# Optimization experiments

Hardware: AMD Instinct MI355X
Metric: run time of the kernel (lower is better)

The kernel has to match this reference:

```python
import jax, jax.numpy as jnp
import numpy as np

B, D_IN, H = 8192, 4096, 128
E, N, C = 3, 256, 32          # experts, codebook_size, codebook_dim
D1, D2 = 512, 256             # down_units
U1, U2 = 256, 512             # up_units
CW = 0.25                     # commitment_weight


def setup_inputs() -> dict:
    key = jax.random.key(0)
    ks = jax.random.split(key, 16)
    s = 0.02
    f32 = jnp.float32
    inp = {
        'x':   jax.random.normal(ks[0], (B, D_IN), f32),
        # llm_down MLP: 4096 -> 512 -> 256 -> 128 (ReLU on hiddens, linear out)
        'Wd1': jax.random.normal(ks[1], (D_IN, D1), f32) * s, 'bd1': jnp.zeros((D1,), f32),
        'Wd2': jax.random.normal(ks[2], (D1, D2), f32) * s,  'bd2': jnp.zeros((D2,), f32),
        'Wd3': jax.random.normal(ks[3], (D2, H), f32) * s,   'bd3': jnp.zeros((H,), f32),
        # per-expert VQ: project_in 128->32, codebook [256,32], project_out 32->128
        'Win':  jax.random.normal(ks[4], (E, H, C), f32) * s, 'bin_': jnp.zeros((E, C), f32),
        'codebook': jax.random.normal(ks[5], (E, N, C), f32),
        'Wout': jax.random.normal(ks[6], (E, C, H), f32) * s, 'bout': jnp.zeros((E, H), f32),
        # llm_up MLP: 128 -> 256 -> 512 -> 4096
        'Wu1': jax.random.normal(ks[7], (H, U1), f32) * s,   'bu1': jnp.zeros((U1,), f32),
        'Wu2': jax.random.normal(ks[8], (U1, U2), f32) * s,  'bu2': jnp.zeros((U2,), f32),
        'Wu3': jax.random.normal(ks[9], (U2, D_IN), f32) * s, 'bu3': jnp.zeros((D_IN,), f32),
    }
    return inp


def _decorrelation_loss(qemb):
    # qemb: [B, E, H]
    b, e, h = qemb.shape
    cen = qemb - qemb.mean(axis=0, keepdims=True)
    cen = cen.transpose(1, 0, 2).reshape(e, -1)          # [E, B*H]
    cov = (cen @ cen.T) / (b * h - 1)                    # [E, E]
    std = jnp.sqrt(jnp.diag(cov))
    std = jnp.where(std > 1e-8, std, 1.0)
    corr = cov / jnp.outer(std, std)
    c2 = corr ** 2
    return c2.sum() - jnp.diag(c2).sum()


def _vq_experts(latent, Win, bin_, codebook, Wout, bout):
    # latent: [B,H]; all experts share the same (unmasked) latent.
    xe = jnp.einsum('bh,ehc->ebc', latent, Win) + bin_[:, None, :]      # [E,B,C]
    d2 = ((xe ** 2).sum(-1)[..., None]
          - 2.0 * jnp.einsum('ebc,enc->ebn', xe, codebook)
          + (codebook ** 2).sum(-1)[:, None, :])                        # [E,B,N]
    idx = jnp.argmin(d2, axis=-1)                                       # [E,B]
    q = jax.vmap(lambda c, i: c[i])(codebook, idx)                      # [E,B,C] gather
    commit = CW * jnp.mean((jax.lax.stop_gradient(q) - xe) ** 2, axis=(1, 2)).sum()
    quant = xe + jax.lax.stop_gradient(q - xe)                          # straight-through
    qe = jnp.einsum('ebc,ech->ebh', quant, Wout) + bout[:, None, :]     # [E,B,H]
    return qe, idx, commit


def reference(x, Wd1, bd1, Wd2, bd2, Wd3, bd3, Win, bin_, codebook, Wout, bout,
              Wu1, bu1, Wu2, bu2, Wu3, bu3):
    h = jax.nn.relu(x @ Wd1 + bd1)
    h = jax.nn.relu(h @ Wd2 + bd2)
    latent = h @ Wd3 + bd3                                              # [B,128]
    qe, idx, total_commit = _vq_experts(latent, Win, bin_, codebook, Wout, bout)
    qemb = qe.transpose(1, 0, 2)                                        # [B,E,H]
    decorr = _decorrelation_loss(qemb)
    rl = qemb.mean(axis=1)                                              # [B,H]
    u = jax.nn.relu(rl @ Wu1 + bu1)
    u = jax.nn.relu(u @ Wu2 + bu2)
    recon = jnp.clip(u @ Wu3 + bu3, -1.0, 1.0)                          # [B,4096]
    return (recon, idx.T, total_commit, decorr)
```

## Files before the change

kernel.cpp:

```cpp
#include <hip/hip_runtime.h>
#include <hip/hip_bf16.h>

using bf16 = __hip_bfloat16;

typedef __bf16 bf16x8 __attribute__((ext_vector_type(8)));
typedef float  f32x4  __attribute__((ext_vector_type(4)));
typedef unsigned long long u64;
typedef unsigned short u16;
typedef unsigned int u32;

__device__ __forceinline__ float b2f(bf16 v) { return __bfloat162float(v); }
__device__ __forceinline__ bf16  f2b(float v) { return __float2bfloat16(v); }
__device__ __forceinline__ u16   bits(bf16 v) { return __builtin_bit_cast(u16, v); }

static constexpr size_t SZ_WD1S = 512ull  * 12288 * 2;
static constexpr size_t SZ_WD2S = 256ull  * 1536  * 2;
static constexpr size_t SZ_WFUS = 128ull  * 768   * 2;
static constexpr size_t SZ_WU1T = 256ull  * 128   * 2;
static constexpr size_t SZ_WU2T = 512ull  * 256   * 2;
static constexpr size_t SZ_WU3T = 4096ull * 512   * 2;
static constexpr size_t SZ_H1S  = 8192ull * 1536  * 2;
static constexpr size_t SZ_H2S  = 8192ull * 768   * 2;
static constexpr size_t SZ_XE   = 8192ull * 128   * 4;
static constexpr size_t SZ_QEMB = 3ull * 8192 * 128 * 4;
static constexpr size_t SZ_RL   = 8192ull * 128   * 2;
static constexpr size_t SZ_U1   = 8192ull * 256   * 2;
static constexpr size_t SZ_U2   = 8192ull * 512   * 2;
static constexpr size_t SZ_CNRM = 768ull * 4;
static constexpr size_t SZ_BFUS = 128ull * 4;
static constexpr size_t SZ_PART = 4ull * 8192 * 512 * 4;

static constexpr size_t OFF_WD1S = 0;
static constexpr size_t OFF_WD2S = OFF_WD1S + SZ_WD1S;
static constexpr size_t OFF_WFUS = OFF_WD2S + SZ_WD2S;
static constexpr size_t OFF_WU1T = OFF_WFUS + SZ_WFUS;
static constexpr size_t OFF_WU2T = OFF_WU1T + SZ_WU1T;
static constexpr size_t OFF_WU3T = OFF_WU2T + SZ_WU2T;
static constexpr size_t OFF_H1S  = OFF_WU3T + SZ_WU3T;
static constexpr size_t OFF_H2S  = OFF_H1S  + SZ_H1S;
static constexpr size_t OFF_XE   = OFF_H2S  + SZ_H2S;
static constexpr size_t OFF_QEMB = OFF_XE   + SZ_XE;
static constexpr size_t OFF_RL   = OFF_QEMB + SZ_QEMB;
static constexpr size_t OFF_U1   = OFF_RL   + SZ_RL;
static constexpr size_t OFF_U2   = OFF_U1   + SZ_U1;
static constexpr size_t OFF_CNRM = OFF_U2   + SZ_U2;
static constexpr size_t OFF_BFUS = OFF_CNRM + ((SZ_CNRM + 255) & ~size_t(255));
static constexpr size_t OFF_STAT = OFF_BFUS + ((SZ_BFUS + 255) & ~size_t(255));
static constexpr size_t OFF_PART = OFF_STAT + 2048;

__global__ void wtrans_bf16(const float* __restrict__ in, bf16* __restrict__ out,
                            int K, int N)
{
    __shared__ float tile[32][33];
    const int tx = threadIdx.x, ty = threadIdx.y;
    const int n0 = blockIdx.x * 32, k0 = blockIdx.y * 32;
    #pragma unroll
    for (int i = 0; i < 32; i += 8)
        tile[ty + i][tx] = in[(size_t)(k0 + ty + i) * N + n0 + tx];
    __syncthreads();
    #pragma unroll
    for (int i = 0; i < 32; i += 8)
        out[(size_t)(n0 + ty + i) * K + k0 + tx] = f2b(tile[tx][ty + i]);
}

__global__ void wtrans_split3(const float* __restrict__ in, bf16* __restrict__ out,
                              int K, int N)
{
    __shared__ float tile[32][33];
    const int tx = threadIdx.x, ty = threadIdx.y;
    const int n0 = blockIdx.x * 32, k0 = blockIdx.y * 32;
    #pragma unroll
    for (int i = 0; i < 32; i += 8)
        tile[ty + i][tx] = in[(size_t)(k0 + ty + i) * N + n0 + tx];
    __syncthreads();
    #pragma unroll
    for (int i = 0; i < 32; i += 8) {
        const float v = tile[tx][ty + i];
        const bf16 hi = f2b(v);
        const bf16 lo = f2b(v - b2f(hi));
        bf16* o = out + (size_t)(n0 + ty + i) * 3 * K + 3 * (k0 + tx);
        o[0] = hi; o[1] = lo; o[2] = hi;
    }
}

__global__ void cnorm_kernel(const float* __restrict__ cb, float* __restrict__ cnorm)
{
    const int i = blockIdx.x * blockDim.x + threadIdx.x;
    if (i < 768) {
        float s = 0.f;
        for (int k = 0; k < 32; ++k) { const float v = cb[i * 32 + k]; s += v * v; }
        cnorm[i] = s;
    }
}

__global__ __launch_bounds__(256)
void wfuse_kernel(const float* __restrict__ Wd3, const float* __restrict__ bd3,
                  const float* __restrict__ Win, const float* __restrict__ bin_,
                  bf16* __restrict__ BtS, float* __restrict__ bfuse)
{
    const int n = blockIdx.x;
    const int t = threadIdx.x;
    if (n >= 96) {
        bf16* o = BtS + (size_t)n * 768 + 3 * t;
        o[0] = f2b(0.f); o[1] = f2b(0.f); o[2] = f2b(0.f);
        if (t == 0) bfuse[n] = 0.f;
        return;
    }
    const int e = n >> 5, c = n & 31;
    float s = 0.f;
    for (int h = 0; h < 128; ++h)
        s += Wd3[t * 128 + h] * Win[(size_t)(e * 128 + h) * 32 + c];
    const bf16 hi = f2b(s);
    const bf16 lo = f2b(s - b2f(hi));
    bf16* o = BtS + (size_t)n * 768 + 3 * t;
    o[0] = hi; o[1] = lo; o[2] = hi;
    if (t == 0) {
        float b = bin_[e * 32 + c];
        for (int h = 0; h < 128; ++h)
            b += bd3[h] * Win[(size_t)(e * 128 + h) * 32 + c];
        bfuse[n] = b;
    }
}

__global__ __launch_bounds__(256)
void gemm1_x3(const float* __restrict__ A, const bf16* __restrict__ Bs3,
              float* __restrict__ part)
{
    __shared__ bf16 As[128 * 96];
    __shared__ bf16 Bs[128 * 96];
    const int t = threadIdx.x, lane = t & 63, w = t >> 6;
    const int n0 = blockIdx.x * 128;
    const int m0 = blockIdx.y * 128;
    const int kz = blockIdx.z;
    const int wr = w >> 1, wc = w & 1, l15 = lane & 15, quad = lane >> 4;

    f32x4 acc[4][4];
    #pragma unroll
    for (int i = 0; i < 4; ++i)
        #pragma unroll
        for (int j = 0; j < 4; ++j)
            #pragma unroll
            for (int r = 0; r < 4; ++r) acc[i][j][r] = 0.f;

    const int kend = kz * 1024 + 1024;
    for (int ko = kz * 1024; ko < kend; ko += 32) {
        #pragma unroll
        for (int i = 0; i < 6; ++i) {
            const int c   = i * 256 + t;
            const int row = c / 12;
            const int cc  = c - row * 12;
            const bf16* gb = Bs3 + (size_t)(n0 + row) * 12288 + ko * 3 + cc * 8;
            __builtin_amdgcn_global_load_lds(
                (const __attribute__((address_space(1))) void*)gb,
                (__attribute__((address_space(3))) void*)(Bs + (size_t)c * 8), 16, 0, 0);
        }
        #pragma unroll
        for (int i = 0; i < 4; ++i) {
            const int c = i * 256 + t;
            const int row = c >> 3, c4 = c & 7;
            const float4 v = *(const float4*)(A + (size_t)(m0 + row) * 4096 + ko + c4 * 4);
            const float va[4] = {v.x, v.y, v.z, v.w};
            u64 h[4], l[4];
            #pragma unroll
            for (int j = 0; j < 4; ++j) {
                const bf16 hh = f2b(va[j]);
                h[j] = bits(hh);
                l[j] = bits(f2b(va[j] - b2f(hh)));
            }
            const u64 p0 = h[0] | (h[0] << 16) | (l[0] << 32) | (h[1] << 48);
            const u64 p1 = h[1] | (l[1] << 16) | (h[2] << 32) | (h[2] << 48);
            const u64 p2 = l[2] | (h[3] << 16) | (h[3] << 32) | (l[3] << 48);
            u64* dst = (u64*)(As + (size_t)row * 96 + c4 * 12);
            dst[0] = p0; dst[1] = p1; dst[2] = p2;
        }
        __syncthreads();
        #pragma unroll
        for (int kk = 0; kk < 3; ++kk) {
            bf16x8 af[4], bfr[4];
            #pragma unroll
            for (int mi = 0; mi < 4; ++mi)
                af[mi] = *(const bf16x8*)(As + (wr * 64 + mi * 16 + l15) * 96 + kk * 32 + quad * 8);
            #pragma unroll
            for (int ni = 0; ni < 4; ++ni)
                bfr[ni] = *(const bf16x8*)(Bs + (wc * 64 + ni * 16 + l15) * 96 + kk * 32 + quad * 8);
            #pragma unroll
            for (int mi = 0; mi < 4; ++mi)
                #pragma unroll
                for (int ni = 0; ni < 4; ++ni)
                    acc[mi][ni] = __builtin_amdgcn_mfma_f32_16x16x32_bf16(
                        af[mi], bfr[ni], acc[mi][ni], 0, 0, 0);
        }
        __syncthreads();
    }

    float* op = part + (size_t)kz * (8192ull * 512);
    #pragma unroll
    for (int mi = 0; mi < 4; ++mi)
        #pragma unroll
        for (int ni = 0; ni < 4; ++ni) {
            const int col = n0 + wc * 64 + ni * 16 + l15;
            #pragma unroll
            for (int r = 0; r < 4; ++r) {
                const int row = m0 + wr * 64 + mi * 16 + quad * 4 + r;
                op[(size_t)row * 512 + col] = acc[mi][ni][r];
            }
        }
}

__global__ __launch_bounds__(256)
void h1_epi(const float* __restrict__ part, const float* __restrict__ bias,
            bf16* __restrict__ out)
{
    const int idx = blockIdx.x * 256 + threadIdx.x;
    const int r = idx >> 7, c4 = idx & 127;
    const size_t base = (size_t)r * 512 + c4 * 4;
    const float4 p0 = *(const float4*)(part + 0ull * 8192 * 512 + base);
    const float4 p1 = *(const float4*)(part + 1ull * 8192 * 512 + base);
    const float4 p2 = *(const float4*)(part + 2ull * 8192 * 512 + base);
    const float4 p3 = *(const float4*)(part + 3ull * 8192 * 512 + base);
    const float4 bv = *(const float4*)(bias + c4 * 4);
    float v[4];
    v[0] = p0.x + p1.x + p2.x + p3.x + bv.x;
    v[1] = p0.y + p1.y + p2.y + p3.y + bv.y;
    v[2] = p0.z + p1.z + p2.z + p3.z + bv.z;
    v[3] = p0.w + p1.w + p2.w + p3.w + bv.w;
    u64 h[4], l[4];
    #pragma unroll
    for (int j = 0; j < 4; ++j) {
        const float vv = v[j] > 0.f ? v[j] : 0.f;
        const bf16 hi = f2b(vv);
        h[j] = bits(hi);
        l[j] = bits(f2b(vv - b2f(hi)));
    }
    const u64 w0 = h[0] | (h[0] << 16) | (l[0] << 32) | (h[1] << 48);
    const u64 w1 = h[1] | (l[1] << 16) | (h[2] << 32) | (h[2] << 48);
    const u64 w2 = l[2] | (h[3] << 16) | (h[3] << 32) | (l[3] << 48);
    u64* dst = (u64*)(out + (size_t)r * 1536 + 12 * c4);
    dst[0] = w0; dst[1] = w1; dst[2] = w2;
}

template <int EPI, int RELU>
__global__ __launch_bounds__(256)
void gemm_bt(const bf16* __restrict__ A, const bf16* __restrict__ Bt,
             const float* __restrict__ bias, void* __restrict__ outp,
             int M, int N, int K)
{
    __shared__ bf16 As[128 * 64];
    __shared__ bf16 Bs[128 * 64];
    const int t = threadIdx.x, lane = t & 63, w = t >> 6;
    const int n0 = blockIdx.x * 128;
    const int m0 = blockIdx.y * 128;
    const int wr = w >> 1, wc = w & 1, l15 = lane & 15, quad = lane >> 4;

    f32x4 acc[4][4];
    #pragma unroll
    for (int i = 0; i < 4; ++i)
        #pragma unroll
        for (int j = 0; j < 4; ++j)
            #pragma unroll
            for (int r = 0; r < 4; ++r) acc[i][j][r] = 0.f;

    for (int k0 = 0; k0 < K; k0 += 64) {
        #pragma unroll
        for (int i = 0; i < 4; ++i) {
            const int c   = i * 256 + t;
            const int row = c >> 3;
            const int col = (c & 7) * 8;
            const bf16* ga = A  + (size_t)(m0 + row) * K + k0 + col;
            const bf16* gb = Bt + (size_t)(n0 + row) * K + k0 + col;
            __builtin_amdgcn_global_load_lds(
                (const __attribute__((address_space(1))) void*)ga,
                (__attribute__((address_space(3))) void*)(As + (size_t)c * 8), 16, 0, 0);
            __builtin_amdgcn_global_load_lds(
                (const __attribute__((address_space(1))) void*)gb,
                (__attribute__((address_space(3))) void*)(Bs + (size_t)c * 8), 16, 0, 0);
        }
        __syncthreads();
        #pragma unroll
        for (int kk = 0; kk < 2; ++kk) {
            bf16x8 af[4], bfr[4];
            #pragma unroll
            for (int mi = 0; mi < 4; ++mi)
                af[mi] = *(const bf16x8*)(As + (wr * 64 + mi * 16 + l15) * 64 + kk * 32 + quad * 8);
            #pragma unroll
            for (int ni = 0; ni < 4; ++ni)
                bfr[ni] = *(const bf16x8*)(Bs + (wc * 64 + ni * 16 + l15) * 64 + kk * 32 + quad * 8);
            #pragma unroll
            for (int mi = 0; mi < 4; ++mi)
                #pragma unroll
                for (int ni = 0; ni < 4; ++ni)
                    acc[mi][ni] = __builtin_amdgcn_mfma_f32_16x16x32_bf16(
                        af[mi], bfr[ni], acc[mi][ni], 0, 0, 0);
        }
        __syncthreads();
    }

    #pragma unroll
    for (int mi = 0; mi < 4; ++mi)
        #pragma unroll
        for (int ni = 0; ni < 4; ++ni) {
            const int col = n0 + wc * 64 + ni * 16 + l15;
            const float bv = bias[col];
            #pragma unroll
            for (int r = 0; r < 4; ++r) {
                const int row = m0 + wr * 64 + mi * 16 + quad * 4 + r;
                float v = acc[mi][ni][r] + bv;
                if (RELU) v = v > 0.f ? v : 0.f;
                if (EPI == 0) {
                    ((float*)outp)[(size_t)row * N + col] = v;
                } else if (EPI == 1) {
                    const bf16 hi = f2b(v);
                    const bf16 lo = f2b(v - b2f(hi));
                    bf16* o = (bf16*)outp + (size_t)row * 3 * N + 3 * col;
                    o[0] = hi; o[1] = hi; o[2] = lo;
                } else if (EPI == 2) {
                    ((bf16*)outp)[(size_t)row * N + col] = f2b(v);
                } else {
                    v = fminf(fmaxf(v, -1.f), 1.f);
                    ((float*)outp)[(size_t)row * N + col] = v;
                }
            }
        }
}

__global__ __launch_bounds__(256)
void vq2_kernel(const float* __restrict__ xe_buf, const float* __restrict__ cb,
                const float* __restrict__ cnorm, const float* __restrict__ Wout,
                const float* __restrict__ bout, float* __restrict__ qemb,
                float* __restrict__ idx_out, float* __restrict__ commit_acc)
{
    __shared__ float cb_s[256 * 36];
    __shared__ float wo_s[32 * 128];
    __shared__ float cn_s[256];
    __shared__ float bo_s[128];
    __shared__ float xe_s[4 * 32];
    __shared__ float q_s[4 * 32];
    __shared__ int   idx_s[4];
    __shared__ u64   wred[4][4];
    __shared__ float cred[256];

    const int e  = blockIdx.x >> 6;
    const int rb = blockIdx.x & 63;
    const int t = threadIdx.x, lane = t & 63, w = t >> 6;

    for (int j = t; j < 256 * 32; j += 256) {
        const int code = j >> 5, c = j & 31;
        cb_s[code * 36 + c] = cb[(size_t)e * 8192 + j];
    }
    for (int j = t; j < 4096; j += 256) wo_s[j] = Wout[(size_t)e * 4096 + j];
    cn_s[t] = cnorm[e * 256 + t];
    if (t < 128) bo_s[t] = bout[e * 128 + t];
    float commit_loc = 0.f;
    __syncthreads();

    for (int it = 0; it < 32; ++it) {
        const int r0 = rb * 128 + it * 4;
        if (t < 128) {
            const int r4 = t >> 5, c = t & 31;
            xe_s[r4 * 32 + c] = xe_buf[(size_t)(r0 + r4) * 128 + e * 32 + c];
        }
        __syncthreads();

        u64 key[4];
        {
            const float4* cp = (const float4*)(cb_s + t * 36);
            const float cn = cn_s[t];
            #pragma unroll
            for (int r4 = 0; r4 < 4; ++r4) {
                float dot = 0.f;
                #pragma unroll
                for (int c4 = 0; c4 < 8; ++c4) {
                    const float4 cv = cp[c4];
                    const float4 xv = *(const float4*)(xe_s + r4 * 32 + c4 * 4);
                    dot += xv.x * cv.x + xv.y * cv.y + xv.z * cv.z + xv.w * cv.w;
                }
                const float d = cn - 2.f * dot;
                u32 ub = __builtin_bit_cast(u32, d);
                ub = (ub & 0x80000000u) ? ~ub : (ub | 0x80000000u);
                key[r4] = ((u64)ub << 32) | (u32)t;
            }
        }
        #pragma unroll
        for (int off = 32; off; off >>= 1) {
            #pragma unroll
            for (int r4 = 0; r4 < 4; ++r4) {
                const u64 o = __shfl_down(key[r4], off, 64);
                if (o < key[r4]) key[r4] = o;
            }
        }
        if (lane == 0) {
            #pragma unroll
            for (int r4 = 0; r4 < 4; ++r4) wred[r4][w] = key[r4];
        }
        __syncthreads();
        if (t < 4) {
            u64 k = wred[t][0];
            #pragma unroll
            for (int ww = 1; ww < 4; ++ww) if (wred[t][ww] < k) k = wred[t][ww];
            const int code = (int)(k & 0xFFFFFFFFu);
            idx_s[t] = code;
            idx_out[(size_t)(r0 + t) * 3 + e] = (float)code;
        }
        __syncthreads();
        if (t < 128) {
            const int r4 = t >> 5, c = t & 31;
            const float q = cb_s[idx_s[r4] * 36 + c];
            q_s[r4 * 32 + c] = q;
            const float dd = q - xe_s[r4 * 32 + c];
            commit_loc += dd * dd;
        }
        __syncthreads();
        #pragma unroll
        for (int p = 0; p < 2; ++p) {
            const int j = p * 256 + t;
            const int r4 = j >> 7, h = j & 127;
            float s = bo_s[h];
            #pragma unroll
            for (int c = 0; c < 32; ++c) s += q_s[r4 * 32 + c] * wo_s[c * 128 + h];
            qemb[((size_t)e * 8192 + r0 + r4) * 128 + h] = s;
        }
        __syncthreads();
    }

    cred[t] = commit_loc;
    __syncthreads();
    for (int o = 128; o; o >>= 1) { if (t < o) cred[t] += cred[t + o]; __syncthreads(); }
    if (t == 0) atomicAdd(commit_acc, cred[0]);
}

__global__ __launch_bounds__(256)
void rlmean_kernel(const float* __restrict__ qemb, bf16* __restrict__ rl,
                   float* __restrict__ meanAcc)
{
    const int t = threadIdx.x, h = t & 127, half = t >> 7;
    const int r0 = blockIdx.x * 64;
    float a0 = 0.f, a1 = 0.f, a2 = 0.f;
    for (int r = r0 + half; r < r0 + 64; r += 2) {
        const float v0 = qemb[((size_t)0 * 8192 + r) * 128 + h];
        const float v1 = qemb[((size_t)1 * 8192 + r) * 128 + h];
        const float v2 = qemb[((size_t)2 * 8192 + r) * 128 + h];
        a0 += v0; a1 += v1; a2 += v2;
        rl[(size_t)r * 128 + h] = f2b((v0 + v1 + v2) * (1.f / 3.f));
    }
    __shared__ float red[3][256];
    red[0][t] = a0; red[1][t] = a1; red[2][t] = a2;
    __syncthreads();
    if (t < 128) {
        atomicAdd(&meanAcc[0 * 128 + h], red[0][t] + red[0][t + 128]);
        atomicAdd(&meanAcc[1 * 128 + h], red[1][t] + red[1][t + 128]);
        atomicAdd(&meanAcc[2 * 128 + h], red[2][t] + red[2][t + 128]);
    }
}

__global__ __launch_bounds__(256)
void gram_kernel(const float* __restrict__ qemb, const float* __restrict__ meanAcc,
                 double* __restrict__ gram)
{
    const int t = threadIdx.x;
    const int h = t & 127, half = t >> 7;
    const int b0 = blockIdx.x * 32;
    const float m0 = meanAcc[0 * 128 + h] * (1.f / 8192.f);
    const float m1 = meanAcc[1 * 128 + h] * (1.f / 8192.f);
    const float m2 = meanAcc[2 * 128 + h] * (1.f / 8192.f);
    float g[6] = {0, 0, 0, 0, 0, 0};
    for (int b = b0 + half; b < b0 + 32; b += 2) {
        const float v0 = qemb[((size_t)0 * 8192 + b) * 128 + h] - m0;
        const float v1 = qemb[((size_t)1 * 8192 + b) * 128 + h] - m1;
        const float v2 = qemb[((size_t)2 * 8192 + b) * 128 + h] - m2;
        g[0] += v0 * v0; g[1] += v0 * v1; g[2] += v0 * v2;
        g[3] += v1 * v1; g[4] += v1 * v2; g[5] += v2 * v2;
    }
    __shared__ float red[256];
    for (int i = 0; i < 6; ++i) {
        red[t] = g[i];
        __syncthreads();
        for (int o = 128; o; o >>= 1) { if (t < o) red[t] += red[t + o]; __syncthreads(); }
        if (t == 0) atomicAdd(&gram[i], (double)red[0]);
        __syncthreads();
    }
}

__global__ void final_kernel(const float* __restrict__ commit_acc,
                             const double* __restrict__ gram,
                             float* __restrict__ out2)
{
    if (threadIdx.x != 0 || blockIdx.x != 0) return;
    const double denom = 8192.0 * 128.0 - 1.0;
    const double c00 = gram[0] / denom, c01 = gram[1] / denom, c02 = gram[2] / denom;
    const double c11 = gram[3] / denom, c12 = gram[4] / denom, c22 = gram[5] / denom;
    double s0 = sqrt(c00), s1 = sqrt(c11), s2 = sqrt(c22);
    if (!(s0 > 1e-8)) s0 = 1.0;
    if (!(s1 > 1e-8)) s1 = 1.0;
    if (!(s2 > 1e-8)) s2 = 1.0;
    const double r01 = c01 / (s0 * s1), r02 = c02 / (s0 * s2), r12 = c12 / (s1 * s2);
    const double decorr = 2.0 * (r01 * r01 + r02 * r02 + r12 * r12);
    out2[0] = (float)((double)commit_acc[0] * (0.25 / (8192.0 * 32.0)));
    out2[1] = (float)decorr;
}

extern "C" void kernel_launch(void* const* d_in, const int* in_sizes, int n_in,
                              void* d_out, int out_size, void* d_ws, size_t ws_size,
                              hipStream_t stream)
{
    const float* x    = (const float*)d_in[0];
    const float* Wd1  = (const float*)d_in[1];
    const float* bd1  = (const float*)d_in[2];
    const float* Wd2  = (const float*)d_in[3];
    const float* bd2  = (const float*)d_in[4];
    const float* Wd3  = (const float*)d_in[5];
    const float* bd3  = (const float*)d_in[6];
    const float* Win  = (const float*)d_in[7];
    const float* bin_ = (const float*)d_in[8];
    const float* cb   = (const float*)d_in[9];
    const float* Wout = (const float*)d_in[10];
    const float* bout = (const float*)d_in[11];
    const float* Wu1  = (const float*)d_in[12];
    const float* bu1  = (const float*)d_in[13];
    const float* Wu2  = (const float*)d_in[14];
    const float* bu2  = (const float*)d_in[15];
    const float* Wu3  = (const float*)d_in[16];
    const float* bu3  = (const float*)d_in[17];

    char* ws = (char*)d_ws;
    bf16*  Wd1s   = (bf16*)(ws + OFF_WD1S);
    bf16*  Wd2s   = (bf16*)(ws + OFF_WD2S);
    bf16*  WfuseS = (bf16*)(ws + OFF_WFUS);
    bf16*  Wu1T   = (bf16*)(ws + OFF_WU1T);
    bf16*  Wu2T   = (bf16*)(ws + OFF_WU2T);
    bf16*  Wu3T   = (bf16*)(ws + OFF_WU3T);
    bf16*  h1s    = (bf16*)(ws + OFF_H1S);
    bf16*  h2s    = (bf16*)(ws + OFF_H2S);
    float* xe     = (float*)(ws + OFF_XE);
    float* qemb   = (float*)(ws + OFF_QEMB);
    bf16*  rl     = (bf16*)(ws + OFF_RL);
    bf16*  u1     = (bf16*)(ws + OFF_U1);
    bf16*  u2     = (bf16*)(ws + OFF_U2);
    float* cnorm  = (float*)(ws + OFF_CNRM);
    float* bfuse  = (float*)(ws + OFF_BFUS);
    float* commit = (float*)(ws + OFF_STAT);
    double* gram  = (double*)(ws + OFF_STAT + 8);
    float* meanA  = (float*)(ws + OFF_STAT + 64);
    float* part   = (float*)(ws + OFF_PART);

    float* out_f   = (float*)d_out;
    float* idx_out = out_f + (size_t)8192 * 4096;
    float* scal    = idx_out + (size_t)8192 * 3;

    hipMemsetAsync(ws + OFF_STAT, 0, 2048, stream);

    const dim3 tb(32, 8);
    wtrans_split3<<<dim3(16, 128), tb, 0, stream>>>(Wd1, Wd1s, 4096, 512);
    wtrans_split3<<<dim3(8, 16),   tb, 0, stream>>>(Wd2, Wd2s, 512, 256);
    wtrans_bf16<<<dim3(8, 4),      tb, 0, stream>>>(Wu1, Wu1T, 128, 256);
    wtrans_bf16<<<dim3(16, 8),     tb, 0, stream>>>(Wu2, Wu2T, 256, 512);
    wtrans_bf16<<<dim3(128, 16),   tb, 0, stream>>>(Wu3, Wu3T, 512, 4096);
    cnorm_kernel<<<3, 256, 0, stream>>>(cb, cnorm);
    wfuse_kernel<<<128, 256, 0, stream>>>(Wd3, bd3, Win, bin_, WfuseS, bfuse);

    gemm1_x3<<<dim3(4, 64, 4), 256, 0, stream>>>(x, Wd1s, part);
    h1_epi<<<4096, 256, 0, stream>>>(part, bd1, h1s);
    gemm_bt<1, 1><<<dim3(2, 64), 256, 0, stream>>>(h1s, Wd2s, bd2, h2s, 8192, 256, 1536);
    gemm_bt<0, 0><<<dim3(1, 64), 256, 0, stream>>>(h2s, WfuseS, bfuse, xe, 8192, 128, 768);

    vq2_kernel<<<192, 256, 0, stream>>>(xe, cb, cnorm, Wout, bout, qemb, idx_out, commit);
    rlmean_kernel<<<128, 256, 0, stream>>>(qemb, rl, meanA);
    gram_kernel<<<256, 256, 0, stream>>>(qemb, meanA, gram);
    final_kernel<<<1, 64, 0, stream>>>(commit, gram, scal);

    gemm_bt<2, 1><<<dim3(2, 64),  256, 0, stream>>>(rl, Wu1T, bu1, u1,    8192, 256,  128);
    gemm_bt<2, 1><<<dim3(4, 64),  256, 0, stream>>>(u1, Wu2T, bu2, u2,    8192, 512,  256);
    gemm_bt<3, 0><<<dim3(32, 64), 256, 0, stream>>>(u2, Wu3T, bu3, out_f, 8192, 4096, 512);

    (void)in_sizes; (void)n_in; (void)out_size; (void)ws_size;
}
```

Measured before the change: 678.0 us.

## Swizzle LDS layouts in GEMMs and cut gemm1 split-K from four to three

Both the split-bf16 first GEMM and the generic bf16 GEMM now use XOR-swizzled shared-memory layouts, so MFMA fragment reads avoid LDS bank conflicts. The first GEMM also restructures its A-tile conversion: each thread loads 16 contiguous floats and writes 128-bit packed hi/lo vectors directly into the swizzled per-kk layout. Split-K drops from 4 to 3 slices (43/43/42 steps), which removes one partial buffer from the epilogue's reduction traffic. The cost is fewer blocks (768) and unequal slices, which may leave some CUs idle.

Result: slower. 704.8 us (+3.9%).

```diff
diff --git a/kernel.cpp b/kernel.cpp
--- a/kernel.cpp
+++ b/kernel.cpp
@@ -5,6 +5,7 @@
 
 typedef __bf16 bf16x8 __attribute__((ext_vector_type(8)));
 typedef float  f32x4  __attribute__((ext_vector_type(4)));
+typedef unsigned int u32x4 __attribute__((ext_vector_type(4)));
 typedef unsigned long long u64;
 typedef unsigned short u16;
 typedef unsigned int u32;
@@ -126,13 +127,14 @@
 void gemm1_x3(const float* __restrict__ A, const bf16* __restrict__ Bs3,
               float* __restrict__ part)
 {
-    __shared__ bf16 As[128 * 96];
-    __shared__ bf16 Bs[128 * 96];
+    __shared__ bf16 As[3 * 4096];
+    __shared__ bf16 Bs[3 * 4096];
     const int t = threadIdx.x, lane = t & 63, w = t >> 6;
     const int n0 = blockIdx.x * 128;
     const int m0 = blockIdx.y * 128;
     const int kz = blockIdx.z;
     const int wr = w >> 1, wc = w & 1, l15 = lane & 15, quad = lane >> 4;
+    const int laneoff = (l15 >> 1) * 64 + (((((l15 & 1) << 2) | quad) ^ ((l15 >> 1) & 7)) << 3);
 
     f32x4 acc[4][4];
     #pragma unroll
@@ -142,36 +144,56 @@
             #pragma unroll
             for (int r = 0; r < 4; ++r) acc[i][j][r] = 0.f;
 
-    const int kend = kz * 1024 + 1024;
-    for (int ko = kz * 1024; ko < kend; ko += 32) {
+    const int arow = t >> 1, ahalf = t & 1;
+    const int ar2 = arow >> 1, arb = (arow & 1) << 2, arx = ar2 & 7;
+
+    int brow[6], bcol[6];
+    #pragma unroll
+    for (int i = 0; i < 6; ++i) {
+        const int p = i * 256 + t;
+        const int bkk = p >> 9, br2 = (p >> 3) & 63;
+        const int c3 = (p & 7) ^ (br2 & 7);
+        brow[i] = 2 * br2 + (c3 >> 2);
+        bcol[i] = bkk * 32 + (c3 & 3) * 8;
+    }
+
+    const int s0 = kz * 43;
+    const int s1 = (kz == 2) ? 128 : (s0 + 43);
+    for (int ks = s0; ks < s1; ++ks) {
+        const int ko = ks * 32;
+        const float* ap = A + (size_t)(m0 + arow) * 4096 + ko + ahalf * 16;
+        float f[16];
+        *(float4*)(f + 0)  = *(const float4*)(ap + 0);
+        *(float4*)(f + 4)  = *(const float4*)(ap + 4);
+        *(float4*)(f + 8)  = *(const float4*)(ap + 8);
+        *(float4*)(f + 12) = *(const float4*)(ap + 12);
         #pragma unroll
         for (int i = 0; i < 6; ++i) {
-            const int c   = i * 256 + t;
-            const int row = c / 12;
-            const int cc  = c - row * 12;
-            const bf16* gb = Bs3 + (size_t)(n0 + row) * 12288 + ko * 3 + cc * 8;
+            const bf16* gb = Bs3 + (size_t)(n0 + brow[i]) * 12288 + ko * 3 + bcol[i];
             __builtin_amdgcn_global_load_lds(
                 (const __attribute__((address_space(1))) void*)gb,
-                (__attribute__((address_space(3))) void*)(Bs + (size_t)c * 8), 16, 0, 0);
-        }
-        #pragma unroll
-        for (int i = 0; i < 4; ++i) {
-            const int c = i * 256 + t;
-            const int row = c >> 3, c4 = c & 7;
-            const float4 v = *(const float4*)(A + (size_t)(m0 + row) * 4096 + ko + c4 * 4);
-            const float va[4] = {v.x, v.y, v.z, v.w};
-            u64 h[4], l[4];
-            #pragma unroll
-            for (int j = 0; j < 4; ++j) {
-                const bf16 hh = f2b(va[j]);
-                h[j] = bits(hh);
-                l[j] = bits(f2b(va[j] - b2f(hh)));
+                (__attribute__((address_space(3))) void*)(Bs + (size_t)(i * 256 + t) * 8), 16, 0, 0);
+        }
+        u32 hi[16], lo[16];
+        #pragma unroll
+        for (int k = 0; k < 16; ++k) {
+            const bf16 hh = f2b(f[k]);
+            hi[k] = bits(hh);
+            lo[k] = bits(f2b(f[k] - b2f(hh)));
+        }
+        #pragma unroll
+        for (int j = 0; j < 6; ++j) {
+            const int cir = ahalf * 6 + j;
+            const int kk = cir >> 2, q = cir & 3;
+            u32x4 wv;
+            #pragma unroll
+            for (int i2 = 0; i2 < 4; ++i2) {
+                const int e0 = j * 8 + i2 * 2, e1 = e0 + 1;
+                const u32 a0 = ((e0 % 3) < 2) ? hi[e0 / 3] : lo[e0 / 3];
+                const u32 a1 = ((e1 % 3) < 2) ? hi[e1 / 3] : lo[e1 / 3];
+                wv[i2] = a0 | (a1 << 16);
             }
-            const u64 p0 = h[0] | (h[0] << 16) | (l[0] << 32) | (h[1] << 48);
-            const u64 p1 = h[1] | (l[1] << 16) | (h[2] << 32) | (h[2] << 48);
-            const u64 p2 = l[2] | (h[3] << 16) | (h[3] << 32) | (l[3] << 48);
-            u64* dst = (u64*)(As + (size_t)row * 96 + c4 * 12);
-            dst[0] = p0; dst[1] = p1; dst[2] = p2;
+            *(u32x4*)(As + kk * 4096 + ar2 * 64 + (((arb | q) ^ arx) << 3)) = wv;
         }
         __syncthreads();
         #pragma unroll
@@ -179,10 +201,10 @@
             bf16x8 af[4], bfr[4];
             #pragma unroll
             for (int mi = 0; mi < 4; ++mi)
-                af[mi] = *(const bf16x8*)(As + (wr * 64 + mi * 16 + l15) * 96 + kk * 32 + quad * 8);
+                af[mi] = *(const bf16x8*)(As + kk * 4096 + wr * 2048 + mi * 512 + laneoff);
             #pragma unroll
             for (int ni = 0; ni < 4; ++ni)
-                bfr[ni] = *(const bf16x8*)(Bs + (wc * 64 + ni * 16 + l15) * 96 + kk * 32 + quad * 8);
+                bfr[ni] = *(const bf16x8*)(Bs + kk * 4096 + wc * 2048 + ni * 512 + laneoff);
             #pragma unroll
             for (int mi = 0; mi < 4; ++mi)
                 #pragma unroll
@@ -217,13 +239,12 @@
     const float4 p0 = *(const float4*)(part + 0ull * 8192 * 512 + base);
     const float4 p1 = *(const float4*)(part + 1ull * 8192 * 512 + base);
     const float4 p2 = *(const float4*)(part + 2ull * 8192 * 512 + base);
-    const float4 p3 = *(const float4*)(part + 3ull * 8192 * 512 + base);
     const float4 bv = *(const float4*)(bias + c4 * 4);
     float v[4];
-    v[0] = p0.x + p1.x + p2.x + p3.x + bv.x;
-    v[1] = p0.y + p1.y + p2.y + p3.y + bv.y;
-    v[2] = p0.z + p1.z + p2.z + p3.z + bv.z;
-    v[3] = p0.w + p1.w + p2.w + p3.w + bv.w;
+    v[0] = p0.x + p1.x + p2.x + bv.x;
+    v[1] = p0.y + p1.y + p2.y + bv.y;
+    v[2] = p0.z + p1.z + p2.z + bv.z;
+    v[3] = p0.w + p1.w + p2.w + bv.w;
     u64 h[4], l[4];
     #pragma unroll
     for (int j = 0; j < 4; ++j) {
@@ -251,6 +272,7 @@
     const int n0 = blockIdx.x * 128;
     const int m0 = blockIdx.y * 128;
     const int wr = w >> 1, wc = w & 1, l15 = lane & 15, quad = lane >> 4;
+    const int l7 = l15 & 7;
 
     f32x4 acc[4][4];
     #pragma unroll
@@ -260,14 +282,20 @@
             #pragma unroll
             for (int r = 0; r < 4; ++r) acc[i][j][r] = 0.f;
 
+    int lrow[4], lcol[4];
+    #pragma unroll
+    for (int i = 0; i < 4; ++i) {
+        const int c = i * 256 + t;
+        lrow[i] = c >> 3;
+        lcol[i] = ((c & 7) ^ (lrow[i] & 7)) * 8;
+    }
+
     for (int k0 = 0; k0 < K; k0 += 64) {
         #pragma unroll
         for (int i = 0; i < 4; ++i) {
-            const int c   = i * 256 + t;
-            const int row = c >> 3;
-            const int col = (c & 7) * 8;
-            const bf16* ga = A  + (size_t)(m0 + row) * K + k0 + col;
-            const bf16* gb = Bt + (size_t)(n0 + row) * K + k0 + col;
+            const int c = i * 256 + t;
+            const bf16* ga = A  + (size_t)(m0 + lrow[i]) * K + k0 + lcol[i];
+            const bf16* gb = Bt + (size_t)(n0 + lrow[i]) * K + k0 + lcol[i];
             __builtin_amdgcn_global_load_lds(
                 (const __attribute__((address_space(1))) void*)ga,
                 (__attribute__((address_space(3))) void*)(As + (size_t)c * 8), 16, 0, 0);
@@ -278,13 +306,14 @@
         __syncthreads();
         #pragma unroll
         for (int kk = 0; kk < 2; ++kk) {
+            const int sw = (((kk << 2) | quad) ^ l7) << 3;
             bf16x8 af[4], bfr[4];
             #pragma unroll
             for (int mi = 0; mi < 4; ++mi)
-                af[mi] = *(const bf16x8*)(As + (wr * 64 + mi * 16 + l15) * 64 + kk * 32 + quad * 8);
+                af[mi] = *(const bf16x8*)(As + (wr * 64 + mi * 16 + l15) * 64 + sw);
             #pragma unroll
             for (int ni = 0; ni < 4; ++ni)
-                bfr[ni] = *(const bf16x8*)(Bs + (wc * 64 + ni * 16 + l15) * 64 + kk * 32 + quad * 8);
+                bfr[ni] = *(const bf16x8*)(Bs + (wc * 64 + ni * 16 + l15) * 64 + sw);
             #pragma unroll
             for (int mi = 0; mi < 4; ++mi)
                 #pragma unroll
@@ -557,7 +586,7 @@
     cnorm_kernel<<<3, 256, 0, stream>>>(cb, cnorm);
     wfuse_kernel<<<128, 256, 0, stream>>>(Wd3, bd3, Win, bin_, WfuseS, bfuse);
 
-    gemm1_x3<<<dim3(4, 64, 4), 256, 0, stream>>>(x, Wd1s, part);
+    gemm1_x3<<<dim3(4, 64, 3), 256, 0, stream>>>(x, Wd1s, part);
     h1_epi<<<4096, 256, 0, stream>>>(part, bd1, h1s);
     gemm_bt<1, 1><<<dim3(2, 64), 256, 0, stream>>>(h1s, Wd2s, bd2, h2s, 8192, 256, 1536);
     gemm_bt<0, 0><<<dim3(1, 64), 256, 0, stream>>>(h2s, WfuseS, bfuse, xe, 8192, 128, 768);
```
